# Kernel tuning notes

Hardware: AMD Instinct MI355X
Metric: run time of the kernel (lower is better)

The kernel has to match this reference:

```python
import jax, jax.numpy as jnp
import numpy as np

B, S, E, FF, Q = 8, 2048, 768, 3072, 8  # batch, seq, embed_dim, ffn_dim, n_qubits


def setup_inputs() -> dict:
    key = jax.random.key(0)
    k_x, k_phi, k_w1, k_w2 = jax.random.split(key, 4)
    x = jax.random.normal(k_x, (B, S, E), dtype=jnp.float32)
    # trainable RY angles (one per qubit), like tq.RY(has_params=True)
    phi = jax.random.normal(k_phi, (Q,), dtype=jnp.float32)
    # linear1: n_qubits -> ffn_dim ; linear2: ffn_dim -> embed_dim (torch layout [out, in])
    w1 = jax.random.normal(k_w1, (FF, Q), dtype=jnp.float32) / np.sqrt(Q).astype(np.float32)
    b1 = jnp.zeros((FF,), dtype=jnp.float32)
    w2 = jax.random.normal(k_w2, (E, FF), dtype=jnp.float32) / np.sqrt(FF).astype(np.float32)
    b2 = jnp.zeros((E,), dtype=jnp.float32)
    return {"x": x, "phi": phi, "w1": w1, "b1": b1, "w2": w2, "b2": b2}


def reference(x, phi, w1, b1, w2, b2):
    # Quantum block (exact closed form): for each token, encoder applies
    # RY(x_i) on wire i, then a trainable RY(phi_i) on wire i. Starting from
    # |0>^Q this is a product state; RY compose additively and
    # <Z> after RY(theta)|0> == cos(theta). MeasureAll(PauliZ) therefore gives:
    n_qubits = phi.shape[0]
    meas = jnp.cos(x[..., :n_qubits] + phi)          # [B, S, Q]
    # dropout is identity in eval mode
    h = jax.nn.relu(jnp.einsum('bsq,fq->bsf', meas, w1) + b1)  # [B, S, FF]
    return jnp.einsum('bsf,ef->bse', h, w2) + b2               # [B, S, E]
```

## Files before the change

### kernel.cpp

```cpp
#include <hip/hip_runtime.h>
#include <hip/hip_bf16.h>
#include <stdint.h>

#define M_TOK 16384
#define E_DIM 768
#define FF_DIM 3072
#define Q_N 8

typedef __attribute__((ext_vector_type(8))) short bf16x8;
typedef __attribute__((ext_vector_type(4))) float f32x4;

__device__ inline unsigned short f2bf(float f) {
  union { float f; unsigned u; } v; v.f = f;
  unsigned r = v.u + 0x7fffu + ((v.u >> 16) & 1u);
  return (unsigned short)(r >> 16);
}

#define H_BLOCKS 1536
#define CVT_BLOCKS 576

__global__ __launch_bounds__(256) void prep_fused(const float* __restrict__ x,
                                                  const float* __restrict__ phi,
                                                  const float* __restrict__ w1,
                                                  const float* __restrict__ b1,
                                                  const float* __restrict__ w2,
                                                  __hip_bfloat16* __restrict__ hout,
                                                  __hip_bfloat16* __restrict__ w2b) {
  if (blockIdx.x >= H_BLOCKS) {
    const int i0 = ((blockIdx.x - H_BLOCKS) * 256 + threadIdx.x) * 16;
    const float4* src = (const float4*)(w2 + i0);
    float4 v0 = src[0], v1 = src[1], v2 = src[2], v3 = src[3];
    uint4 o0, o1;
    o0.x = (uint32_t)f2bf(v0.x) | ((uint32_t)f2bf(v0.y) << 16);
    o0.y = (uint32_t)f2bf(v0.z) | ((uint32_t)f2bf(v0.w) << 16);
    o0.z = (uint32_t)f2bf(v1.x) | ((uint32_t)f2bf(v1.y) << 16);
    o0.w = (uint32_t)f2bf(v1.z) | ((uint32_t)f2bf(v1.w) << 16);
    o1.x = (uint32_t)f2bf(v2.x) | ((uint32_t)f2bf(v2.y) << 16);
    o1.y = (uint32_t)f2bf(v2.z) | ((uint32_t)f2bf(v2.w) << 16);
    o1.z = (uint32_t)f2bf(v3.x) | ((uint32_t)f2bf(v3.y) << 16);
    o1.w = (uint32_t)f2bf(v3.z) | ((uint32_t)f2bf(v3.w) << 16);
    uint4* dst = (uint4*)((unsigned short*)w2b + i0);
    dst[0] = o0;
    dst[1] = o1;
    return;
  }

  __shared__ float s_meas[32][8];
  const int t = threadIdx.x;
  const int bm = blockIdx.x / 3;
  const int bf = blockIdx.x % 3;
  const int m0 = bm * 32;
  const int f0 = bf * 1024;

  if (t < 64) {
    int m = t >> 1, hh = t & 1;
    float4 v = *(const float4*)(x + (size_t)(m0 + m) * E_DIM + hh * 4);
    float4 p = *(const float4*)(phi + hh * 4);
    s_meas[m][hh * 4 + 0] = __cosf(v.x + p.x);
    s_meas[m][hh * 4 + 1] = __cosf(v.y + p.y);
    s_meas[m][hh * 4 + 2] = __cosf(v.z + p.z);
    s_meas[m][hh * 4 + 3] = __cosf(v.w + p.w);
  }
  __syncthreads();

  const float4* wrp = (const float4*)(w1 + (size_t)(f0 + 4 * t) * Q_N);
  float4 wv[8];
#pragma unroll
  for (int j = 0; j < 8; ++j) wv[j] = wrp[j];
  const float4 bias4 = *(const float4*)(b1 + f0 + 4 * t);

  unsigned short* hbase = (unsigned short*)hout + f0 + 4 * t;
  for (int m = 0; m < 32; ++m) {
    float mvv[8];
#pragma unroll
    for (int q = 0; q < 8; ++q) mvv[q] = s_meas[m][q];
    float a0 = bias4.x, a1 = bias4.y, a2 = bias4.z, a3 = bias4.w;
    a0 = fmaf(mvv[0], wv[0].x, a0); a0 = fmaf(mvv[1], wv[0].y, a0);
    a0 = fmaf(mvv[2], wv[0].z, a0); a0 = fmaf(mvv[3], wv[0].w, a0);
    a0 = fmaf(mvv[4], wv[1].x, a0); a0 = fmaf(mvv[5], wv[1].y, a0);
    a0 = fmaf(mvv[6], wv[1].z, a0); a0 = fmaf(mvv[7], wv[1].w, a0);
    a1 = fmaf(mvv[0], wv[2].x, a1); a1 = fmaf(mvv[1], wv[2].y, a1);
    a1 = fmaf(mvv[2], wv[2].z, a1); a1 = fmaf(mvv[3], wv[2].w, a1);
    a1 = fmaf(mvv[4], wv[3].x, a1); a1 = fmaf(mvv[5], wv[3].y, a1);
    a1 = fmaf(mvv[6], wv[3].z, a1); a1 = fmaf(mvv[7], wv[3].w, a1);
    a2 = fmaf(mvv[0], wv[4].x, a2); a2 = fmaf(mvv[1], wv[4].y, a2);
    a2 = fmaf(mvv[2], wv[4].z, a2); a2 = fmaf(mvv[3], wv[4].w, a2);
    a2 = fmaf(mvv[4], wv[5].x, a2); a2 = fmaf(mvv[5], wv[5].y, a2);
    a2 = fmaf(mvv[6], wv[5].z, a2); a2 = fmaf(mvv[7], wv[5].w, a2);
    a3 = fmaf(mvv[0], wv[6].x, a3); a3 = fmaf(mvv[1], wv[6].y, a3);
    a3 = fmaf(mvv[2], wv[6].z, a3); a3 = fmaf(mvv[3], wv[6].w, a3);
    a3 = fmaf(mvv[4], wv[7].x, a3); a3 = fmaf(mvv[5], wv[7].y, a3);
    a3 = fmaf(mvv[6], wv[7].z, a3); a3 = fmaf(mvv[7], wv[7].w, a3);
    a0 = fmaxf(a0, 0.f); a1 = fmaxf(a1, 0.f);
    a2 = fmaxf(a2, 0.f); a3 = fmaxf(a3, 0.f);
    uint2 pv;
    pv.x = (uint32_t)f2bf(a0) | ((uint32_t)f2bf(a1) << 16);
    pv.y = (uint32_t)f2bf(a2) | ((uint32_t)f2bf(a3) << 16);
    *(uint2*)(hbase + (size_t)(m0 + m) * FF_DIM) = pv;
  }
}

#define GLDS16(g, l)                                                          \
  __builtin_amdgcn_global_load_lds(                                           \
      (const __attribute__((address_space(1))) void*)(g),                     \
      (__attribute__((address_space(3))) void*)(l), 16, 0, 0)

#define BUF_ELEMS 28672
#define B_OFF 16384

__global__ __launch_bounds__(512, 1) void gemm_bt(const __hip_bfloat16* __restrict__ A,
                                                  const __hip_bfloat16* __restrict__ Bw,
                                                  const float* __restrict__ b2,
                                                  float* __restrict__ C) {
  const int K = FF_DIM;
  const int N = E_DIM;

  __shared__ __align__(16) __hip_bfloat16 lds[2 * BUF_ELEMS];

  const int t = threadIdx.x;
  const int swz = (blockIdx.x & 7) * 32 + (blockIdx.x >> 3);
  const int bm = swz >> 2;
  const int bn = swz & 3;
  const size_t m0 = (size_t)bm * 256;
  const int n0 = bn * 192;

  const int w = t >> 6, l = t & 63;
  const int wr = w >> 1;
  const int wc = w & 1;
  const int lr = l & 15;
  const int lk = l >> 4;

  const int x0 = lk ^ (lr & 7);
  const int x1 = x0 ^ 4;
  const int baseA = (wr * 64 + lr) * 64;
  const int baseB = B_OFF + (wc * 96 + lr) * 64;
  const int offA0 = baseA + x0 * 8, offA1 = baseA + x1 * 8;
  const int offB0 = baseB + x0 * 8, offB1 = baseB + x1 * 8;

  const int rs = t >> 3;
  const int lc = (t & 7) ^ (rs & 7);
  const __hip_bfloat16* sA[4];
  const __hip_bfloat16* sB[3];
#pragma unroll
  for (int s = 0; s < 4; ++s) sA[s] = A + (m0 + s * 64 + rs) * (size_t)K + lc * 8;
#pragma unroll
  for (int s = 0; s < 3; ++s) sB[s] = Bw + ((size_t)n0 + s * 64 + rs) * K + lc * 8;

  f32x4 acc[4][6] = {};

#define STAGE(K0S, WBUF)                                                      \
  {                                                                           \
    __hip_bfloat16* ld = lds + (WBUF) * BUF_ELEMS + t * 8;                    \
    GLDS16(sA[0] + (K0S), ld);                                                \
    GLDS16(sA[1] + (K0S), ld + 4096);                                         \
    GLDS16(sA[2] + (K0S), ld + 8192);                                         \
    GLDS16(sA[3] + (K0S), ld + 12288);                                        \
    GLDS16(sB[0] + (K0S), ld + 16384);                                        \
    GLDS16(sB[1] + (K0S), ld + 20480);                                        \
    GLDS16(sB[2] + (K0S), ld + 24576);                                        \
  }

#define TILE(KT, RBUF, DO_STAGE)                                              \
  {                                                                           \
    if (DO_STAGE) STAGE(((KT) + 1) * 64, (RBUF) ^ 1);                         \
    const __hip_bfloat16* la = lds + (RBUF) * BUF_ELEMS;                      \
    {                                                 \
      bf16x8 fa[4], fb[6];                                                    \
      _Pragma("unroll") for (int mi = 0; mi < 4; ++mi)                        \
          fa[mi] = *(const bf16x8*)(la + offA0 + mi * 1024);                  \
      _Pragma("unroll") for (int ni = 0; ni < 6; ++ni)                        \
          fb[ni] = *(const bf16x8*)(la + offB0 + ni * 1024);                  \
      __builtin_amdgcn_s_setprio(1);                                          \
      _Pragma("unroll") for (int mi = 0; mi < 4; ++mi)                        \
          _Pragma("unroll") for (int ni = 0; ni < 6; ++ni)                    \
              acc[mi][ni] = __builtin_amdgcn_mfma_f32_16x16x32_bf16(          \
                  fa[mi], fb[ni], acc[mi][ni], 0, 0, 0);                      \
      __builtin_amdgcn_s_setprio(0);                                          \
    }                                                                         \
    {                                                 \
      bf16x8 fa[4], fb[6];                                                    \
      _Pragma("unroll") for (int mi = 0; mi < 4; ++mi)                        \
          fa[mi] = *(const bf16x8*)(la + offA1 + mi * 1024);                  \
      _Pragma("unroll") for (int ni = 0; ni < 6; ++ni)                        \
          fb[ni] = *(const bf16x8*)(la + offB1 + ni * 1024);                  \
      __builtin_amdgcn_s_setprio(1);                                          \
      _Pragma("unroll") for (int mi = 0; mi < 4; ++mi)                        \
          _Pragma("unroll") for (int ni = 0; ni < 6; ++ni)                    \
              acc[mi][ni] = __builtin_amdgcn_mfma_f32_16x16x32_bf16(          \
                  fa[mi], fb[ni], acc[mi][ni], 0, 0, 0);                      \
      __builtin_amdgcn_s_setprio(0);                                          \
    }                                                                         \
    asm volatile("s_waitcnt vmcnt(0)" ::: "memory");                          \
    __builtin_amdgcn_s_barrier();                                             \
  }

  STAGE(0, 0);
  asm volatile("s_waitcnt vmcnt(0)" ::: "memory");
  __builtin_amdgcn_s_barrier();

#pragma unroll 1
  for (int tt = 0; tt < 46; tt += 2) {
    TILE(tt + 0, 0, 1);
    TILE(tt + 1, 1, 1);
  }
  TILE(46, 0, 1);
  TILE(47, 1, 0);

#undef TILE
#undef STAGE

#pragma unroll
  for (int mi = 0; mi < 4; ++mi) {
    const size_t row = m0 + wr * 64 + mi * 16 + lk * 4;
#pragma unroll
    for (int ni = 0; ni < 6; ++ni) {
      const int col = n0 + wc * 96 + ni * 16 + lr;
      const float bias = b2[col];
#pragma unroll
      for (int rr = 0; rr < 4; ++rr) {
        C[(row + rr) * N + col] = acc[mi][ni][rr] + bias;
      }
    }
  }
}

__global__ __launch_bounds__(256) void fallback_fused(const float* __restrict__ x,
                                                      const float* __restrict__ phi,
                                                      const float* __restrict__ w1,
                                                      const float* __restrict__ b1,
                                                      const float* __restrict__ w2,
                                                      const float* __restrict__ b2,
                                                      float* __restrict__ out) {
  __shared__ float s_h[FF_DIM];
  __shared__ float s_meas[Q_N];
  const int t = threadIdx.x;
  const size_t m = blockIdx.x;
  if (t < Q_N) s_meas[t] = __cosf(x[m * E_DIM + t] + phi[t]);
  __syncthreads();
  for (int f = t; f < FF_DIM; f += 256) {
    const float4* wr = (const float4*)(w1 + (size_t)f * Q_N);
    float4 a = wr[0], b = wr[1];
    float acc = b1[f];
    acc = fmaf(s_meas[0], a.x, acc); acc = fmaf(s_meas[1], a.y, acc);
    acc = fmaf(s_meas[2], a.z, acc); acc = fmaf(s_meas[3], a.w, acc);
    acc = fmaf(s_meas[4], b.x, acc); acc = fmaf(s_meas[5], b.y, acc);
    acc = fmaf(s_meas[6], b.z, acc); acc = fmaf(s_meas[7], b.w, acc);
    s_h[f] = fmaxf(acc, 0.f);
  }
  __syncthreads();
  for (int e = t; e < E_DIM; e += 256) {
    const float* w2r = w2 + (size_t)e * FF_DIM;
    float acc = b2[e];
    for (int f = 0; f < FF_DIM; f += 4) {
      float4 wv = *(const float4*)(w2r + f);
      acc = fmaf(s_h[f + 0], wv.x, acc);
      acc = fmaf(s_h[f + 1], wv.y, acc);
      acc = fmaf(s_h[f + 2], wv.z, acc);
      acc = fmaf(s_h[f + 3], wv.w, acc);
    }
    out[m * E_DIM + e] = acc;
  }
}

extern "C" void kernel_launch(void* const* d_in, const int* in_sizes, int n_in,
                              void* d_out, int out_size, void* d_ws, size_t ws_size,
                              hipStream_t stream) {
  const float* x   = (const float*)d_in[0];
  const float* phi = (const float*)d_in[1];
  const float* w1  = (const float*)d_in[2];
  const float* b1  = (const float*)d_in[3];
  const float* w2  = (const float*)d_in[4];
  const float* b2  = (const float*)d_in[5];
  float* out = (float*)d_out;

  const size_t H_BYTES   = (size_t)M_TOK * FF_DIM * 2;
  const size_t W2B_BYTES = (size_t)E_DIM * FF_DIM * 2;
  const size_t NEED = H_BYTES + W2B_BYTES;

  if (ws_size >= NEED) {
    __hip_bfloat16* h   = (__hip_bfloat16*)d_ws;
    __hip_bfloat16* w2b = (__hip_bfloat16*)((char*)d_ws + H_BYTES);
    prep_fused<<<H_BLOCKS + CVT_BLOCKS, 256, 0, stream>>>(x, phi, w1, b1, w2,
                                                          h, w2b);
    gemm_bt<<<(M_TOK / 256) * (E_DIM / 192), 512, 0, stream>>>(h, w2b, b2, out);
  } else {
    fallback_fused<<<M_TOK, 256, 0, stream>>>(x, phi, w1, b1, w2, b2, out);
  }
}
```

Measured before the change: 95.58 us.

## Merge prep and GEMM into one cooperative kernel with grid sync

Replaces the two-launch sequence (prep_fused producing bf16 H and bf16 W2, then gemm_bt) with a single cooperative kernel of 256 persistent blocks. Each block converts a slice of W2, computes its 64 rows of the hidden activations, hits a grid-wide barrier, then runs the same GEMM body. This aims to remove one kernel launch and the gap between kernels. The cost is a grid sync, and the prep phase now runs at 256 blocks of 512 threads instead of the wider original grid. If the cooperative launch fails it falls back to the two-kernel path.

```diff
diff --git a/kernel.cpp b/kernel.cpp
--- a/kernel.cpp
+++ b/kernel.cpp
@@ -1,6 +1,9 @@
 #include <hip/hip_runtime.h>
 #include <hip/hip_bf16.h>
+#include <hip/hip_cooperative_groups.h>
 #include <stdint.h>
+
+namespace cg = cooperative_groups;
 
 #define M_TOK 16384
 #define E_DIM 768
@@ -16,90 +19,6 @@
   return (unsigned short)(r >> 16);
 }
 
-#define H_BLOCKS 1536
-#define CVT_BLOCKS 576
-
-__global__ __launch_bounds__(256) void prep_fused(const float* __restrict__ x,
-                                                  const float* __restrict__ phi,
-                                                  const float* __restrict__ w1,
-                                                  const float* __restrict__ b1,
-                                                  const float* __restrict__ w2,
-                                                  __hip_bfloat16* __restrict__ hout,
-                                                  __hip_bfloat16* __restrict__ w2b) {
-  if (blockIdx.x >= H_BLOCKS) {
-    const int i0 = ((blockIdx.x - H_BLOCKS) * 256 + threadIdx.x) * 16;
-    const float4* src = (const float4*)(w2 + i0);
-    float4 v0 = src[0], v1 = src[1], v2 = src[2], v3 = src[3];
-    uint4 o0, o1;
-    o0.x = (uint32_t)f2bf(v0.x) | ((uint32_t)f2bf(v0.y) << 16);
-    o0.y = (uint32_t)f2bf(v0.z) | ((uint32_t)f2bf(v0.w) << 16);
-    o0.z = (uint32_t)f2bf(v1.x) | ((uint32_t)f2bf(v1.y) << 16);
-    o0.w = (uint32_t)f2bf(v1.z) | ((uint32_t)f2bf(v1.w) << 16);
-    o1.x = (uint32_t)f2bf(v2.x) | ((uint32_t)f2bf(v2.y) << 16);
-    o1.y = (uint32_t)f2bf(v2.z) | ((uint32_t)f2bf(v2.w) << 16);
-    o1.z = (uint32_t)f2bf(v3.x) | ((uint32_t)f2bf(v3.y) << 16);
-    o1.w = (uint32_t)f2bf(v3.z) | ((uint32_t)f2bf(v3.w) << 16);
-    uint4* dst = (uint4*)((unsigned short*)w2b + i0);
-    dst[0] = o0;
-    dst[1] = o1;
-    return;
-  }
-
-  __shared__ float s_meas[32][8];
-  const int t = threadIdx.x;
-  const int bm = blockIdx.x / 3;
-  const int bf = blockIdx.x % 3;
-  const int m0 = bm * 32;
-  const int f0 = bf * 1024;
-
-  if (t < 64) {
-    int m = t >> 1, hh = t & 1;
-    float4 v = *(const float4*)(x + (size_t)(m0 + m) * E_DIM + hh * 4);
-    float4 p = *(const float4*)(phi + hh * 4);
-    s_meas[m][hh * 4 + 0] = __cosf(v.x + p.x);
-    s_meas[m][hh * 4 + 1] = __cosf(v.y + p.y);
-    s_meas[m][hh * 4 + 2] = __cosf(v.z + p.z);
-    s_meas[m][hh * 4 + 3] = __cosf(v.w + p.w);
-  }
-  __syncthreads();
-
-  const float4* wrp = (const float4*)(w1 + (size_t)(f0 + 4 * t) * Q_N);
-  float4 wv[8];
-#pragma unroll
-  for (int j = 0; j < 8; ++j) wv[j] = wrp[j];
-  const float4 bias4 = *(const float4*)(b1 + f0 + 4 * t);
-
-  unsigned short* hbase = (unsigned short*)hout + f0 + 4 * t;
-  for (int m = 0; m < 32; ++m) {
-    float mvv[8];
-#pragma unroll
-    for (int q = 0; q < 8; ++q) mvv[q] = s_meas[m][q];
-    float a0 = bias4.x, a1 = bias4.y, a2 = bias4.z, a3 = bias4.w;
-    a0 = fmaf(mvv[0], wv[0].x, a0); a0 = fmaf(mvv[1], wv[0].y, a0);
-    a0 = fmaf(mvv[2], wv[0].z, a0); a0 = fmaf(mvv[3], wv[0].w, a0);
-    a0 = fmaf(mvv[4], wv[1].x, a0); a0 = fmaf(mvv[5], wv[1].y, a0);
-    a0 = fmaf(mvv[6], wv[1].z, a0); a0 = fmaf(mvv[7], wv[1].w, a0);
-    a1 = fmaf(mvv[0], wv[2].x, a1); a1 = fmaf(mvv[1], wv[2].y, a1);
-    a1 = fmaf(mvv[2], wv[2].z, a1); a1 = fmaf(mvv[3], wv[2].w, a1);
-    a1 = fmaf(mvv[4], wv[3].x, a1); a1 = fmaf(mvv[5], wv[3].y, a1);
-    a1 = fmaf(mvv[6], wv[3].z, a1); a1 = fmaf(mvv[7], wv[3].w, a1);
-    a2 = fmaf(mvv[0], wv[4].x, a2); a2 = fmaf(mvv[1], wv[4].y, a2);
-    a2 = fmaf(mvv[2], wv[4].z, a2); a2 = fmaf(mvv[3], wv[4].w, a2);
-    a2 = fmaf(mvv[4], wv[5].x, a2); a2 = fmaf(mvv[5], wv[5].y, a2);
-    a2 = fmaf(mvv[6], wv[5].z, a2); a2 = fmaf(mvv[7], wv[5].w, a2);
-    a3 = fmaf(mvv[0], wv[6].x, a3); a3 = fmaf(mvv[1], wv[6].y, a3);
-    a3 = fmaf(mvv[2], wv[6].z, a3); a3 = fmaf(mvv[3], wv[6].w, a3);
-    a3 = fmaf(mvv[4], wv[7].x, a3); a3 = fmaf(mvv[5], wv[7].y, a3);
-    a3 = fmaf(mvv[6], wv[7].z, a3); a3 = fmaf(mvv[7], wv[7].w, a3);
-    a0 = fmaxf(a0, 0.f); a1 = fmaxf(a1, 0.f);
-    a2 = fmaxf(a2, 0.f); a3 = fmaxf(a3, 0.f);
-    uint2 pv;
-    pv.x = (uint32_t)f2bf(a0) | ((uint32_t)f2bf(a1) << 16);
-    pv.y = (uint32_t)f2bf(a2) | ((uint32_t)f2bf(a3) << 16);
-    *(uint2*)(hbase + (size_t)(m0 + m) * FF_DIM) = pv;
-  }
-}
-
 #define GLDS16(g, l)                                                          \
   __builtin_amdgcn_global_load_lds(                                           \
       (const __attribute__((address_space(1))) void*)(g),                     \
@@ -108,17 +27,16 @@
 #define BUF_ELEMS 28672
 #define B_OFF 16384
 
-__global__ __launch_bounds__(512, 1) void gemm_bt(const __hip_bfloat16* __restrict__ A,
-                                                  const __hip_bfloat16* __restrict__ Bw,
-                                                  const float* __restrict__ b2,
-                                                  float* __restrict__ C) {
+__device__ __forceinline__ void gemm_body(const __hip_bfloat16* __restrict__ A,
+                                          const __hip_bfloat16* __restrict__ Bw,
+                                          const float* __restrict__ b2,
+                                          float* __restrict__ C,
+                                          __hip_bfloat16* lds,
+                                          const int t, const int bid) {
   const int K = FF_DIM;
   const int N = E_DIM;
 
-  __shared__ __align__(16) __hip_bfloat16 lds[2 * BUF_ELEMS];
-
-  const int t = threadIdx.x;
-  const int swz = (blockIdx.x & 7) * 32 + (blockIdx.x >> 3);
+  const int swz = (bid & 7) * 32 + (bid >> 3);
   const int bm = swz >> 2;
   const int bn = swz & 3;
   const size_t m0 = (size_t)bm * 256;
@@ -224,6 +142,188 @@
   }
 }
 
+__global__ __launch_bounds__(512, 1) void mega_ffn(const float* __restrict__ x,
+                                                   const float* __restrict__ phi,
+                                                   const float* __restrict__ w1,
+                                                   const float* __restrict__ b1,
+                                                   const float* __restrict__ w2,
+                                                   const float* __restrict__ b2,
+                                                   __hip_bfloat16* __restrict__ hout,
+                                                   __hip_bfloat16* __restrict__ w2b,
+                                                   float* __restrict__ C) {
+  __shared__ __align__(16) __hip_bfloat16 lds[2 * BUF_ELEMS];
+  const int t = threadIdx.x;
+  const int blk = blockIdx.x;
+
+  {
+    const size_t n = (size_t)E_DIM * FF_DIM;
+    const size_t stride = (size_t)256 * 512 * 8;
+    for (size_t i = ((size_t)blk * 512 + t) * 8; i < n; i += stride) {
+      float4 v0 = *(const float4*)(w2 + i);
+      float4 v1 = *(const float4*)(w2 + i + 4);
+      uint4 o;
+      o.x = (uint32_t)f2bf(v0.x) | ((uint32_t)f2bf(v0.y) << 16);
+      o.y = (uint32_t)f2bf(v0.z) | ((uint32_t)f2bf(v0.w) << 16);
+      o.z = (uint32_t)f2bf(v1.x) | ((uint32_t)f2bf(v1.y) << 16);
+      o.w = (uint32_t)f2bf(v1.z) | ((uint32_t)f2bf(v1.w) << 16);
+      *(uint4*)((unsigned short*)w2b + i) = o;
+    }
+  }
+
+  {
+    float* s_meas = (float*)lds;
+    const int m0b = blk * 64;
+    if (t < 128) {
+      int m = t >> 1, hh = t & 1;
+      float4 v = *(const float4*)(x + (size_t)(m0b + m) * E_DIM + hh * 4);
+      float4 p = *(const float4*)(phi + hh * 4);
+      s_meas[m * 8 + hh * 4 + 0] = __cosf(v.x + p.x);
+      s_meas[m * 8 + hh * 4 + 1] = __cosf(v.y + p.y);
+      s_meas[m * 8 + hh * 4 + 2] = __cosf(v.z + p.z);
+      s_meas[m * 8 + hh * 4 + 3] = __cosf(v.w + p.w);
+    }
+    __syncthreads();
+
+    const int tsub = t & 255;
+    const int rt = t >> 8;
+#pragma unroll 1
+    for (int bf = 0; bf < 3; ++bf) {
+      const int f0 = bf * 1024 + 4 * tsub;
+      const float4* wrp = (const float4*)(w1 + (size_t)f0 * Q_N);
+      float4 wv[8];
+#pragma unroll
+      for (int j = 0; j < 8; ++j) wv[j] = wrp[j];
+      const float4 bias4 = *(const float4*)(b1 + f0);
+      unsigned short* hbase = (unsigned short*)hout + f0;
+      for (int m = 0; m < 32; ++m) {
+        const int mloc = rt * 32 + m;
+        float mvv[8];
+#pragma unroll
+        for (int q = 0; q < 8; ++q) mvv[q] = s_meas[mloc * 8 + q];
+        float a0 = bias4.x, a1 = bias4.y, a2 = bias4.z, a3 = bias4.w;
+        a0 = fmaf(mvv[0], wv[0].x, a0); a0 = fmaf(mvv[1], wv[0].y, a0);
+        a0 = fmaf(mvv[2], wv[0].z, a0); a0 = fmaf(mvv[3], wv[0].w, a0);
+        a0 = fmaf(mvv[4], wv[1].x, a0); a0 = fmaf(mvv[5], wv[1].y, a0);
+        a0 = fmaf(mvv[6], wv[1].z, a0); a0 = fmaf(mvv[7], wv[1].w, a0);
+        a1 = fmaf(mvv[0], wv[2].x, a1); a1 = fmaf(mvv[1], wv[2].y, a1);
+        a1 = fmaf(mvv[2], wv[2].z, a1); a1 = fmaf(mvv[3], wv[2].w, a1);
+        a1 = fmaf(mvv[4], wv[3].x, a1); a1 = fmaf(mvv[5], wv[3].y, a1);
+        a1 = fmaf(mvv[6], wv[3].z, a1); a1 = fmaf(mvv[7], wv[3].w, a1);
+        a2 = fmaf(mvv[0], wv[4].x, a2); a2 = fmaf(mvv[1], wv[4].y, a2);
+        a2 = fmaf(mvv[2], wv[4].z, a2); a2 = fmaf(mvv[3], wv[4].w, a2);
+        a2 = fmaf(mvv[4], wv[5].x, a2); a2 = fmaf(mvv[5], wv[5].y, a2);
+        a2 = fmaf(mvv[6], wv[5].z, a2); a2 = fmaf(mvv[7], wv[5].w, a2);
+        a3 = fmaf(mvv[0], wv[6].x, a3); a3 = fmaf(mvv[1], wv[6].y, a3);
+        a3 = fmaf(mvv[2], wv[6].z, a3); a3 = fmaf(mvv[3], wv[6].w, a3);
+        a3 = fmaf(mvv[4], wv[7].x, a3); a3 = fmaf(mvv[5], wv[7].y, a3);
+        a3 = fmaf(mvv[6], wv[7].z, a3); a3 = fmaf(mvv[7], wv[7].w, a3);
+        a0 = fmaxf(a0, 0.f); a1 = fmaxf(a1, 0.f);
+        a2 = fmaxf(a2, 0.f); a3 = fmaxf(a3, 0.f);
+        uint2 pv;
+        pv.x = (uint32_t)f2bf(a0) | ((uint32_t)f2bf(a1) << 16);
+        pv.y = (uint32_t)f2bf(a2) | ((uint32_t)f2bf(a3) << 16);
+        *(uint2*)(hbase + (size_t)(m0b + mloc) * FF_DIM) = pv;
+      }
+    }
+  }
+
+  cg::this_grid().sync();
+
+  gemm_body(hout, w2b, b2, C, lds, t, blk);
+}
+
+#define H_BLOCKS 1536
+#define CVT_BLOCKS 576
+
+__global__ __launch_bounds__(256) void prep_fused(const float* __restrict__ x,
+                                                  const float* __restrict__ phi,
+                                                  const float* __restrict__ w1,
+                                                  const float* __restrict__ b1,
+                                                  const float* __restrict__ w2,
+                                                  __hip_bfloat16* __restrict__ hout,
+                                                  __hip_bfloat16* __restrict__ w2b) {
+  if (blockIdx.x >= H_BLOCKS) {
+    const int i0 = ((blockIdx.x - H_BLOCKS) * 256 + threadIdx.x) * 16;
+    const float4* src = (const float4*)(w2 + i0);
+    float4 v0 = src[0], v1 = src[1], v2 = src[2], v3 = src[3];
+    uint4 o0, o1;
+    o0.x = (uint32_t)f2bf(v0.x) | ((uint32_t)f2bf(v0.y) << 16);
+    o0.y = (uint32_t)f2bf(v0.z) | ((uint32_t)f2bf(v0.w) << 16);
+    o0.z = (uint32_t)f2bf(v1.x) | ((uint32_t)f2bf(v1.y) << 16);
+    o0.w = (uint32_t)f2bf(v1.z) | ((uint32_t)f2bf(v1.w) << 16);
+    o1.x = (uint32_t)f2bf(v2.x) | ((uint32_t)f2bf(v2.y) << 16);
+    o1.y = (uint32_t)f2bf(v2.z) | ((uint32_t)f2bf(v2.w) << 16);
+    o1.z = (uint32_t)f2bf(v3.x) | ((uint32_t)f2bf(v3.y) << 16);
+    o1.w = (uint32_t)f2bf(v3.z) | ((uint32_t)f2bf(v3.w) << 16);
+    uint4* dst = (uint4*)((unsigned short*)w2b + i0);
+    dst[0] = o0;
+    dst[1] = o1;
+    return;
+  }
+
+  __shared__ float s_meas[32][8];
+  const int t = threadIdx.x;
+  const int bm = blockIdx.x / 3;
+  const int bf = blockIdx.x % 3;
+  const int m0 = bm * 32;
+  const int f0 = bf * 1024;
+
+  if (t < 64) {
+    int m = t >> 1, hh = t & 1;
+    float4 v = *(const float4*)(x + (size_t)(m0 + m) * E_DIM + hh * 4);
+    float4 p = *(const float4*)(phi + hh * 4);
+    s_meas[m][hh * 4 + 0] = __cosf(v.x + p.x);
+    s_meas[m][hh * 4 + 1] = __cosf(v.y + p.y);
+    s_meas[m][hh * 4 + 2] = __cosf(v.z + p.z);
+    s_meas[m][hh * 4 + 3] = __cosf(v.w + p.w);
+  }
+  __syncthreads();
+
+  const float4* wrp = (const float4*)(w1 + (size_t)(f0 + 4 * t) * Q_N);
+  float4 wv[8];
+#pragma unroll
+  for (int j = 0; j < 8; ++j) wv[j] = wrp[j];
+  const float4 bias4 = *(const float4*)(b1 + f0 + 4 * t);
+
+  unsigned short* hbase = (unsigned short*)hout + f0 + 4 * t;
+  for (int m = 0; m < 32; ++m) {
+    float mvv[8];
+#pragma unroll
+    for (int q = 0; q < 8; ++q) mvv[q] = s_meas[m][q];
+    float a0 = bias4.x, a1 = bias4.y, a2 = bias4.z, a3 = bias4.w;
+    a0 = fmaf(mvv[0], wv[0].x, a0); a0 = fmaf(mvv[1], wv[0].y, a0);
+    a0 = fmaf(mvv[2], wv[0].z, a0); a0 = fmaf(mvv[3], wv[0].w, a0);
+    a0 = fmaf(mvv[4], wv[1].x, a0); a0 = fmaf(mvv[5], wv[1].y, a0);
+    a0 = fmaf(mvv[6], wv[1].z, a0); a0 = fmaf(mvv[7], wv[1].w, a0);
+    a1 = fmaf(mvv[0], wv[2].x, a1); a1 = fmaf(mvv[1], wv[2].y, a1);
+    a1 = fmaf(mvv[2], wv[2].z, a1); a1 = fmaf(mvv[3], wv[2].w, a1);
+    a1 = fmaf(mvv[4], wv[3].x, a1); a1 = fmaf(mvv[5], wv[3].y, a1);
+    a1 = fmaf(mvv[6], wv[3].z, a1); a1 = fmaf(mvv[7], wv[3].w, a1);
+    a2 = fmaf(mvv[0], wv[4].x, a2); a2 = fmaf(mvv[1], wv[4].y, a2);
+    a2 = fmaf(mvv[2], wv[4].z, a2); a2 = fmaf(mvv[3], wv[4].w, a2);
+    a2 = fmaf(mvv[4], wv[5].x, a2); a2 = fmaf(mvv[5], wv[5].y, a2);
+    a2 = fmaf(mvv[6], wv[5].z, a2); a2 = fmaf(mvv[7], wv[5].w, a2);
+    a3 = fmaf(mvv[0], wv[6].x, a3); a3 = fmaf(mvv[1], wv[6].y, a3);
+    a3 = fmaf(mvv[2], wv[6].z, a3); a3 = fmaf(mvv[3], wv[6].w, a3);
+    a3 = fmaf(mvv[4], wv[7].x, a3); a3 = fmaf(mvv[5], wv[7].y, a3);
+    a3 = fmaf(mvv[6], wv[7].z, a3); a3 = fmaf(mvv[7], wv[7].w, a3);
+    a0 = fmaxf(a0, 0.f); a1 = fmaxf(a1, 0.f);
+    a2 = fmaxf(a2, 0.f); a3 = fmaxf(a3, 0.f);
+    uint2 pv;
+    pv.x = (uint32_t)f2bf(a0) | ((uint32_t)f2bf(a1) << 16);
+    pv.y = (uint32_t)f2bf(a2) | ((uint32_t)f2bf(a3) << 16);
+    *(uint2*)(hbase + (size_t)(m0 + m) * FF_DIM) = pv;
+  }
+}
+
+__global__ __launch_bounds__(512, 1) void gemm_bt(const __hip_bfloat16* __restrict__ A,
+                                                  const __hip_bfloat16* __restrict__ Bw,
+                                                  const float* __restrict__ b2,
+                                                  float* __restrict__ C) {
+  __shared__ __align__(16) __hip_bfloat16 lds[2 * BUF_ELEMS];
+  gemm_body(A, Bw, b2, C, lds, threadIdx.x, blockIdx.x);
+}
+
 __global__ __launch_bounds__(256) void fallback_fused(const float* __restrict__ x,
                                                       const float* __restrict__ phi,
                                                       const float* __restrict__ w1,
@@ -280,9 +380,18 @@
   if (ws_size >= NEED) {
     __hip_bfloat16* h   = (__hip_bfloat16*)d_ws;
     __hip_bfloat16* w2b = (__hip_bfloat16*)((char*)d_ws + H_BYTES);
-    prep_fused<<<H_BLOCKS + CVT_BLOCKS, 256, 0, stream>>>(x, phi, w1, b1, w2,
-                                                          h, w2b);
-    gemm_bt<<<(M_TOK / 256) * (E_DIM / 192), 512, 0, stream>>>(h, w2b, b2, out);
+
+    void* args[] = {(void*)&x, (void*)&phi, (void*)&w1, (void*)&b1,
+                    (void*)&w2, (void*)&b2, (void*)&h, (void*)&w2b,
+                    (void*)&out};
+    hipError_t err = hipLaunchCooperativeKernel(
+        (const void*)mega_ffn, dim3(256), dim3(512), args, 0, stream);
+    if (err != hipSuccess) {
+      prep_fused<<<H_BLOCKS + CVT_BLOCKS, 256, 0, stream>>>(x, phi, w1, b1, w2,
+                                                            h, w2b);
+      gemm_bt<<<(M_TOK / 256) * (E_DIM / 192), 512, 0, stream>>>(h, w2b, b2,
+                                                                 out);
+    }
   } else {
     fallback_fused<<<M_TOK, 256, 0, stream>>>(x, phi, w1, b1, w2, b2, out);
   }
```

Result: slower. 134.5 us (+40.7%).
